# Optimization experiments

Hardware: AMD Instinct MI355X
Metric: run time of the kernel (lower is better)

Reference implementation:

```python
import jax, jax.numpy as jnp
import numpy as np

KERNEL_SIZE = 3  # init kwarg
METRIC = 'MSE'   # init kwarg


def setup_inputs() -> dict:
    key = jax.random.key(0)
    k1, k2, k3 = jax.random.split(key, 3)
    B, H, W, S = 16, 2048, 2048, 5000
    predictions = jax.random.normal(k1, (B, 1, H, W), dtype=jnp.float32)
    # pos[...,0] = px in [0,W), pos[...,1] = py in [0,H)
    station_positions = jax.random.randint(k2, (B, S, 2), 0, 2048, dtype=jnp.int32)
    station_runoffs = jax.random.normal(k3, (B, S), dtype=jnp.float32)
    return {
        'predictions': predictions,
        'station_positions': station_positions,
        'station_runoffs': station_runoffs,
    }


def reference(predictions, station_positions, station_runoffs):
    B, _, H, W = predictions.shape
    kh = KERNEL_SIZE // 2
    # kernel offsets, flattened to (K2,)
    offs = jnp.arange(-kh, kh + 1)
    dy, dx = jnp.meshgrid(offs, offs, indexing='ij')
    dy = dy.reshape(-1)
    dx = dx.reshape(-1)
    px = station_positions[..., 0]  # (B,S) -> width index
    py = station_positions[..., 1]  # (B,S) -> height index
    ys = py[..., None] + dy  # (B,S,K2)
    xs = px[..., None] + dx  # (B,S,K2)
    valid = (ys >= 0) & (ys < H) & (xs >= 0) & (xs < W)
    ysc = jnp.clip(ys, 0, H - 1)
    xsc = jnp.clip(xs, 0, W - 1)
    b_idx = jnp.arange(B)[:, None, None]
    vals = predictions[b_idx, 0, ysc, xsc]  # (B,S,K2) gathered neighborhoods
    validf = valid.astype(predictions.dtype)
    counts = validf.sum(-1)  # >=4 always (corner of 3x3 window)
    avg_pred = (vals * validf).sum(-1) / counts  # (B,S) per-station window mean
    if METRIC == 'MSE':
        per_station = (avg_pred - station_runoffs) ** 2
    else:  # MAE
        per_station = jnp.abs(avg_pred - station_runoffs)
    # original: sum of per-station losses / num_stations
    return jnp.mean(per_station)
```

## Files before the change

### kernel.cpp

```cpp
#include <hip/hip_runtime.h>


#define BB 16
#define HH 2048
#define WW 2048
#define SS 5000
#define NSTATIONS (BB * SS)
#define THREADS 256
#define NBLOCKS ((NSTATIONS + THREADS - 1) / THREADS)

__global__ __launch_bounds__(THREADS) void station_partial_kernel(
    const float* __restrict__ pred,
    const int2*  __restrict__ pos,
    const float* __restrict__ runoff,
    float* __restrict__ partials)
{
    int t = blockIdx.x * blockDim.x + threadIdx.x;
    float contrib = 0.0f;
    if (t < NSTATIONS) {
        int b = t / SS;
        int2 p = pos[t];
        int px = p.x;
        int py = p.y;
        const float* img = pred + (size_t)b * (size_t)(HH * WW);

        float sum = 0.0f;
        float cnt = 0.0f;
        #pragma unroll
        for (int dy = -1; dy <= 1; ++dy) {
            int y = py + dy;
            bool yok = (y >= 0) & (y < HH);
            int yc = min(max(y, 0), HH - 1);
            const float* row = img + (size_t)yc * WW;
            #pragma unroll
            for (int dx = -1; dx <= 1; ++dx) {
                int x = px + dx;
                bool ok = yok & (x >= 0) & (x < WW);
                int xc = min(max(x, 0), WW - 1);
                float v = row[xc];
                float m = ok ? 1.0f : 0.0f;
                sum += v * m;
                cnt += m;
            }
        }
        float avg = sum / cnt;
        float d = avg - runoff[t];
        contrib = d * d;
    }

    #pragma unroll
    for (int off = 32; off > 0; off >>= 1)
        contrib += __shfl_down(contrib, off, 64);

    __shared__ float waves[THREADS / 64];
    int lane = threadIdx.x & 63;
    int wid  = threadIdx.x >> 6;
    if (lane == 0) waves[wid] = contrib;
    __syncthreads();
    if (threadIdx.x == 0) {
        float s = 0.0f;
        #pragma unroll
        for (int i = 0; i < THREADS / 64; ++i) s += waves[i];
        partials[blockIdx.x] = s;
    }
}

__global__ __launch_bounds__(512) void reduce_kernel(
    const float* __restrict__ partials, float* __restrict__ out)
{
    float v = 0.0f;
    for (int i = threadIdx.x; i < NBLOCKS; i += 512) v += partials[i];
    #pragma unroll
    for (int off = 32; off > 0; off >>= 1)
        v += __shfl_down(v, off, 64);

    __shared__ float waves[512 / 64];
    int lane = threadIdx.x & 63;
    int wid  = threadIdx.x >> 6;
    if (lane == 0) waves[wid] = v;
    __syncthreads();
    if (threadIdx.x == 0) {
        float s = 0.0f;
        #pragma unroll
        for (int i = 0; i < 512 / 64; ++i) s += waves[i];
        out[0] = s * (1.0f / (float)NSTATIONS);
    }
}

extern "C" void kernel_launch(void* const* d_in, const int* in_sizes, int n_in,
                              void* d_out, int out_size, void* d_ws, size_t ws_size,
                              hipStream_t stream) {
    const float* pred   = (const float*)d_in[0];
    const int2*  pos    = (const int2*)d_in[1];
    const float* runoff = (const float*)d_in[2];
    float* out      = (float*)d_out;
    float* partials = (float*)d_ws;

    station_partial_kernel<<<NBLOCKS, THREADS, 0, stream>>>(pred, pos, runoff, partials);
    reduce_kernel<<<1, 512, 0, stream>>>(partials, out);
}
```

Baseline: 307.2 us.

## Bucket-sort stations by image region before gathering neighborhoods

Adds a counting sort of stations into spatial buckets (per batch, groups of 8 rows by half-width) with histogram, scan and atomic scatter kernels. The gather kernel then reads stations in sorted order, so neighboring threads touch nearby rows and cache lines, and runoff is packed alongside each position. The cost being targeted is scattered, uncoalesced reads of the 3x3 windows across a large image. In exchange it adds four extra launches, global atomics and a serial single-block scan.

```diff
diff --git a/kernel.cpp b/kernel.cpp
--- a/kernel.cpp
+++ b/kernel.cpp
@@ -7,21 +7,83 @@
 #define SS 5000
 #define NSTATIONS (BB * SS)
 #define THREADS 256
-#define NBLOCKS ((NSTATIONS + THREADS - 1) / THREADS)
+#define NB_STATION ((NSTATIONS + THREADS - 1) / THREADS)
+#define NBUCKETS 8192
 
-__global__ __launch_bounds__(THREADS) void station_partial_kernel(
-    const float* __restrict__ pred,
-    const int2*  __restrict__ pos,
-    const float* __restrict__ runoff,
+
+__device__ __forceinline__ int bucket_of(int b, int px, int py) {
+    return (b << 9) | ((py >> 3) << 1) | (px >> 10);
+}
+
+__global__ __launch_bounds__(THREADS) void zero_hist(unsigned int* __restrict__ hist) {
+    int t = blockIdx.x * blockDim.x + threadIdx.x;
+    if (t < NBUCKETS) hist[t] = 0u;
+}
+
+__global__ __launch_bounds__(THREADS) void hist_kernel(
+    const int2* __restrict__ pos, unsigned int* __restrict__ hist)
+{
+    int t = blockIdx.x * blockDim.x + threadIdx.x;
+    if (t < NSTATIONS) {
+        int b = t / SS;
+        int2 p = pos[t];
+        atomicAdd(&hist[bucket_of(b, p.x, p.y)], 1u);
+    }
+}
+
+__global__ __launch_bounds__(1024) void scan_kernel(unsigned int* __restrict__ hist)
+{
+    __shared__ unsigned int sums[1024];
+    int t = threadIdx.x;
+    unsigned int local[8];
+    unsigned int s = 0;
+    #pragma unroll
+    for (int i = 0; i < 8; ++i) { local[i] = hist[t * 8 + i]; s += local[i]; }
+    sums[t] = s;
+    __syncthreads();
+    for (int off = 1; off < 1024; off <<= 1) {
+        unsigned int v = (t >= off) ? sums[t - off] : 0u;
+        __syncthreads();
+        sums[t] += v;
+        __syncthreads();
+    }
+    unsigned int base = sums[t] - s;
+    #pragma unroll
+    for (int i = 0; i < 8; ++i) {
+        unsigned int c = local[i];
+        hist[t * 8 + i] = base;
+        base += c;
+    }
+}
+
+__global__ __launch_bounds__(THREADS) void scatter_kernel(
+    const int2* __restrict__ pos, const float* __restrict__ runoff,
+    unsigned int* __restrict__ hist, uint2* __restrict__ sorted)
+{
+    int t = blockIdx.x * blockDim.x + threadIdx.x;
+    if (t < NSTATIONS) {
+        int b = t / SS;
+        int2 p = pos[t];
+        float r = runoff[t];
+        unsigned int idx = atomicAdd(&hist[bucket_of(b, p.x, p.y)], 1u);
+        unsigned int packed = (unsigned int)p.x | ((unsigned int)p.y << 11)
+                            | ((unsigned int)b << 22);
+        sorted[idx] = make_uint2(packed, __float_as_uint(r));
+    }
+}
+
+__global__ __launch_bounds__(THREADS) void gather_kernel(
+    const float* __restrict__ pred, const uint2* __restrict__ sorted,
     float* __restrict__ partials)
 {
     int t = blockIdx.x * blockDim.x + threadIdx.x;
     float contrib = 0.0f;
     if (t < NSTATIONS) {
-        int b = t / SS;
-        int2 p = pos[t];
-        int px = p.x;
-        int py = p.y;
+        uint2 rec = sorted[t];
+        int px = (int)(rec.x & 2047u);
+        int py = (int)((rec.x >> 11) & 2047u);
+        int b  = (int)(rec.x >> 22);
+        float ro = __uint_as_float(rec.y);
         const float* img = pred + (size_t)b * (size_t)(HH * WW);
 
         float sum = 0.0f;
@@ -44,7 +106,7 @@
             }
         }
         float avg = sum / cnt;
-        float d = avg - runoff[t];
+        float d = avg - ro;
         contrib = d * d;
     }
 
@@ -69,7 +131,7 @@
     const float* __restrict__ partials, float* __restrict__ out)
 {
     float v = 0.0f;
-    for (int i = threadIdx.x; i < NBLOCKS; i += 512) v += partials[i];
+    for (int i = threadIdx.x; i < NB_STATION; i += 512) v += partials[i];
     #pragma unroll
     for (int off = 32; off > 0; off >>= 1)
         v += __shfl_down(v, off, 64);
@@ -93,9 +155,17 @@
     const float* pred   = (const float*)d_in[0];
     const int2*  pos    = (const int2*)d_in[1];
     const float* runoff = (const float*)d_in[2];
-    float* out      = (float*)d_out;
-    float* partials = (float*)d_ws;
+    float* out = (float*)d_out;
 
-    station_partial_kernel<<<NBLOCKS, THREADS, 0, stream>>>(pred, pos, runoff, partials);
+    char* ws = (char*)d_ws;
+    unsigned int* hist  = (unsigned int*)(ws);
+    float* partials     = (float*)(ws + 32768);
+    uint2* sorted       = (uint2*)(ws + 36864);
+
+    zero_hist<<<NBUCKETS / THREADS, THREADS, 0, stream>>>(hist);
+    hist_kernel<<<NB_STATION, THREADS, 0, stream>>>(pos, hist);
+    scan_kernel<<<1, 1024, 0, stream>>>(hist);
+    scatter_kernel<<<NB_STATION, THREADS, 0, stream>>>(pos, runoff, hist, sorted);
+    gather_kernel<<<NB_STATION, THREADS, 0, stream>>>(pred, sorted, partials);
     reduce_kernel<<<1, 512, 0, stream>>>(partials, out);
 }
```

After: 321.8 us. 4.8% more time.
